# Performance work log

Hardware: AMD Instinct MI355X
Metric: run time of the kernel (lower is better)

Reference implementation:

```python
import jax, jax.numpy as jnp
import numpy as np

B, L, D_MODEL = 4, 1024, 512
D_STATE, EXPAND, D_CONV = 16, 2, 4
D_INNER = EXPAND * D_MODEL
DT_RANK = D_MODEL // 16
NUM_LAYERS = 2
NL2 = 2 * NUM_LAYERS  # at/vt layer pairs, index 2*i -> at_i, 2*i+1 -> vt_i


def setup_inputs() -> dict:
    key = jax.random.key(0)
    ks = jax.random.split(key, 16)
    s = 0.02
    inp = {
        'a_x': jax.random.normal(ks[0], (B, L, D_MODEL), jnp.float32),
        'v_x': jax.random.normal(ks[1], (B, L, D_MODEL), jnp.float32),
        't_x': jax.random.normal(ks[2], (B, L, D_MODEL), jnp.float32),
        'in_proj_w': s * jax.random.normal(ks[3], (NL2, 2 * D_INNER, D_MODEL), jnp.float32),
        'conv_w': s * jax.random.normal(ks[4], (NL2, 2, D_INNER, D_CONV), jnp.float32),
        'conv_b': jnp.zeros((NL2, 2, D_INNER), jnp.float32),
        'xproj_w': s * jax.random.normal(ks[5], (NL2, 2, DT_RANK + 2 * D_STATE, D_INNER), jnp.float32),
        'dtproj_w': s * jax.random.normal(ks[6], (NL2, 2, D_INNER, DT_RANK), jnp.float32),
        'dtproj_b': 0.1 * jax.random.normal(ks[7], (NL2, 2, D_INNER), jnp.float32),
        'A_log': jnp.log(jnp.broadcast_to(jnp.arange(1.0, D_STATE + 1.0, dtype=jnp.float32), (NL2, 2, D_INNER, D_STATE))),
        'Dskip': jnp.ones((NL2, 2, D_INNER), jnp.float32),
        'out_proj_w': s * jax.random.normal(ks[8], (NL2, D_MODEL, D_INNER), jnp.float32),
        'ln_w': jnp.ones((NL2, 2, D_MODEL), jnp.float32),
        'ln_b': jnp.zeros((NL2, 2, D_MODEL), jnp.float32),
    }
    return inp


def layer_norm(x, w, b, eps=1e-6):
    m = jnp.mean(x, -1, keepdims=True)
    v = jnp.var(x, -1, keepdims=True)
    return (x - m) * jax.lax.rsqrt(v + eps) * w + b


def causal_conv1d(x, w, b):
    # x: (B,L,d), depthwise causal conv with kernel w: (d,k), bias b: (d,)
    y = jax.lax.conv_general_dilated(
        x.transpose(0, 2, 1), w[:, None, :], (1,), [(D_CONV - 1, 0)],
        feature_group_count=D_INNER,
        dimension_numbers=('NCH', 'OIH', 'NCH'))
    return y.transpose(0, 2, 1) + b


def selective_scan(u, dt, A, Bm, Cm, Dskip):
    # u,dt:(B,L,d)  A:(d,N)  Bm,Cm:(B,L,N)  Dskip:(d,)
    dA = jnp.exp(dt[..., None] * A)                    # (B,L,d,N)
    dBu = (dt * u)[..., None] * Bm[:, :, None, :]      # (B,L,d,N)

    def step(h, inp):
        dA_t, dBu_t, C_t = inp
        h = dA_t * h + dBu_t                           # (B,d,N)
        return h, jnp.einsum('bdn,bn->bd', h, C_t)

    h0 = jnp.zeros((u.shape[0], u.shape[2], D_STATE), u.dtype)
    xs = (jnp.moveaxis(dA, 1, 0), jnp.moveaxis(dBu, 1, 0), jnp.moveaxis(Cm, 1, 0))
    _, ys = jax.lax.scan(step, h0, xs)
    return jnp.moveaxis(ys, 0, 1) + u * Dskip


def _one_dir(x, cw, cb, xpw, dpw, dpb, A_log, Dskip):
    xc = jax.nn.silu(causal_conv1d(x, cw, cb))
    proj = xc @ xpw.T                                  # (B,L,dt_rank+2N)
    dt_r, Bm, Cm = jnp.split(proj, [DT_RANK, DT_RANK + D_STATE], axis=-1)
    dt = jax.nn.softplus(dt_r @ dpw.T + dpb)
    A = -jnp.exp(A_log)
    return selective_scan(xc, dt, A, Bm, Cm, Dskip)


def _bimamba(u, i, p):
    xz = u @ p['in_proj_w'][i].T
    x, z = jnp.split(xz, 2, axis=-1)
    yf = _one_dir(x, p['conv_w'][i, 0], p['conv_b'][i, 0], p['xproj_w'][i, 0],
                  p['dtproj_w'][i, 0], p['dtproj_b'][i, 0], p['A_log'][i, 0], p['Dskip'][i, 0])
    yb = _one_dir(x[:, ::-1], p['conv_w'][i, 1], p['conv_b'][i, 1], p['xproj_w'][i, 1],
                  p['dtproj_w'][i, 1], p['dtproj_b'][i, 1], p['A_log'][i, 1], p['Dskip'][i, 1])[:, ::-1]
    y = (yf + yb) * jax.nn.silu(z)
    return y @ p['out_proj_w'][i].T


def _enc_layer(a, t, i, p):
    ao = _bimamba(a, i, p)
    to = _bimamba(t, i, p)
    a_out = a + layer_norm(ao, p['ln_w'][i, 0], p['ln_b'][i, 0])
    t_out = t + layer_norm(to, p['ln_w'][i, 1], p['ln_b'][i, 1])
    return a_out, t_out


def reference(a_x, v_x, t_x, in_proj_w, conv_w, conv_b, xproj_w, dtproj_w, dtproj_b,
              A_log, Dskip, out_proj_w, ln_w, ln_b):
    p = dict(in_proj_w=in_proj_w, conv_w=conv_w, conv_b=conv_b, xproj_w=xproj_w,
             dtproj_w=dtproj_w, dtproj_b=dtproj_b, A_log=A_log, Dskip=Dskip,
             out_proj_w=out_proj_w, ln_w=ln_w, ln_b=ln_b)
    a_out, v_out, t_out = a_x, v_x, t_x
    for i in range(NUM_LAYERS):
        a_out, t_at = _enc_layer(a_out, t_out, 2 * i, p)
        v_out, t_vt = _enc_layer(v_out, t_out, 2 * i + 1, p)
        t_out = (t_at + t_vt) / 2
    return (a_out, v_out, t_out)
```

## Files before the change

### kernel.cpp

```cpp
#include <hip/hip_runtime.h>
#include <cstddef>

constexpr int B_      = 4;
constexpr int L_      = 1024;
constexpr int DM      = 512;
constexpr int DS      = 16;
constexpr int DI      = 1024;
constexpr int DTR     = 32;
constexpr int TOK     = B_ * L_;
constexpr int NLAYERS = 2;

constexpr size_t XZB = 0;
constexpr size_t XCB = (size_t)4 * TOK * 2 * DI * 2;
constexpr size_t PRB = XCB + (size_t)8 * TOK * DI * 2;
constexpr size_t WIB = PRB + (size_t)8 * TOK * 64 * 4;
constexpr size_t WOB = WIB + (size_t)4 * 2 * DI * DM * 2;
constexpr size_t WXB = WOB + (size_t)4 * DM * DI * 2;
constexpr size_t WS_NEED_BF = WXB + (size_t)8 * 64 * DI * 2;
constexpr size_t DTB2 = WS_NEED_BF;
constexpr size_t WS_NEED_DT = DTB2 + (size_t)8 * TOK * DI * 2;

constexpr int NCH = 16;
constexpr size_t PP_BYTE = (size_t)8 * 4 * NCH * 1024 * DS * 2;

#if defined(__has_builtin)
#if __has_builtin(__builtin_amdgcn_exp2f)
#define FAST_EXP2(x) __builtin_amdgcn_exp2f(x)
#endif
#endif
#ifndef FAST_EXP2
#define FAST_EXP2(x) exp2f(x)
#endif

__device__ __forceinline__ float silu_f(float x) { return x / (1.f + __expf(-x)); }

__device__ __forceinline__ float bf2f(unsigned short u) {
    union { unsigned u; float f; } v; v.u = ((unsigned)u) << 16; return v.f;
}
__device__ __forceinline__ unsigned short f2bf(float f) {
    union { float f; unsigned u; } v; v.f = f;
    unsigned r = v.u + 0x7FFFu + ((v.u >> 16) & 1u);
    return (unsigned short)(r >> 16);
}
__device__ __forceinline__ float softplus_f(float x) {
    float e = exp2f(-fabsf(x) * 1.44269504f);
    return fmaxf(x, 0.f) + 0.69314718f * log2f(1.f + e);
}

__device__ __forceinline__ size_t ovmap(size_t byte) {
    return ((byte >> 11) << 12) + (byte & 2047);
}
__device__ __forceinline__ void st4bf(char* b, size_t bank, size_t e, float4 v) {
    ushort4 o;
    o.x = f2bf(v.x); o.y = f2bf(v.y); o.z = f2bf(v.z); o.w = f2bf(v.w);
    *(ushort4*)(b + ovmap(bank + e * 2)) = o;
}
__device__ __forceinline__ float4 ld4bf(const char* b, size_t bank, size_t e) {
    ushort4 u = *(const ushort4*)(b + ovmap(bank + e * 2));
    return make_float4(bf2f(u.x), bf2f(u.y), bf2f(u.z), bf2f(u.w));
}

using bf16x8 = __attribute__((ext_vector_type(8))) short;
using f32x4v = __attribute__((ext_vector_type(4))) float;
using f32x2  = __attribute__((ext_vector_type(2))) float;

__device__ __forceinline__ void stage8(unsigned short* dst, const float* src) {
    float4 v0 = *(const float4*)src;
    float4 v1 = *(const float4*)(src + 4);
    ushort4 o0, o1;
    o0.x = f2bf(v0.x); o0.y = f2bf(v0.y); o0.z = f2bf(v0.z); o0.w = f2bf(v0.w);
    o1.x = f2bf(v1.x); o1.y = f2bf(v1.y); o1.z = f2bf(v1.z); o1.w = f2bf(v1.w);
    *(ushort4*)dst = o0;
    *(ushort4*)(dst + 4) = o1;
}
__device__ __forceinline__ void stage8(unsigned short* dst, const unsigned short* src) {
    *(uint4*)dst = *(const uint4*)src;
}

template<int N, int K, int LDKA, int BM, int BN, int FM, int FN, int EPI,
         typename TA, typename TW, typename TC>
__device__ __forceinline__ void mfma_gemm(const TA* __restrict__ A,
                                          const TW* __restrict__ W,
                                          TC* __restrict__ C,
                                          const float* __restrict__ bias)
{
    constexpr int WC  = BN / (FN * 16);
    constexpr int LDA = 40;
    __shared__ unsigned short As[BM * LDA];
    __shared__ unsigned short Bs[BN * LDA];
    const int tid  = threadIdx.x;
    const int lane = tid & 63, wid = tid >> 6;
    const int wr = wid / WC, wc = wid % WC;
    const int row0 = blockIdx.y * BM, col0 = blockIdx.x * BN;

    f32x4v acc[FM][FN] = {};
    constexpr int AITER = BM * 4 / 256;
    constexpr int BITER = BN * 4 / 256;

    for (int k0 = 0; k0 < K; k0 += 32) {
#pragma unroll
        for (int i = 0; i < AITER; ++i) {
            int f = i * 256 + tid;
            int row = f >> 2, c8 = (f & 3) * 8;
            stage8(&As[row * LDA + c8], A + (size_t)(row0 + row) * LDKA + k0 + c8);
        }
#pragma unroll
        for (int i = 0; i < BITER; ++i) {
            int f = i * 256 + tid;
            int row = f >> 2, c8 = (f & 3) * 8;
            stage8(&Bs[row * LDA + c8], W + (size_t)(col0 + row) * K + k0 + c8);
        }
        __syncthreads();
        bf16x8 af[FM], bfr[FN];
#pragma unroll
        for (int m = 0; m < FM; ++m)
            af[m] = *(const bf16x8*)&As[(wr * FM * 16 + m * 16 + (lane & 15)) * LDA + (lane >> 4) * 8];
#pragma unroll
        for (int n = 0; n < FN; ++n)
            bfr[n] = *(const bf16x8*)&Bs[(wc * FN * 16 + n * 16 + (lane & 15)) * LDA + (lane >> 4) * 8];
#pragma unroll
        for (int m = 0; m < FM; ++m)
#pragma unroll
            for (int n = 0; n < FN; ++n)
                acc[m][n] = __builtin_amdgcn_mfma_f32_16x16x32_bf16(af[m], bfr[n], acc[m][n], 0, 0, 0);
        __syncthreads();
    }
#pragma unroll
    for (int m = 0; m < FM; ++m) {
#pragma unroll
        for (int n = 0; n < FN; ++n) {
            int r0 = row0 + wr * FM * 16 + m * 16 + (lane >> 4) * 4;
            int c  = col0 + wc * FN * 16 + n * 16 + (lane & 15);
#pragma unroll
            for (int v = 0; v < 4; ++v) {
                float val = acc[m][n][v];
                if constexpr (EPI == 1) val = softplus_f(val + bias[c]);
                if constexpr (sizeof(TC) == 4)
                    C[(size_t)(r0 + v) * N + c] = val;
                else
                    C[(size_t)(r0 + v) * N + c] = f2bf(val);
            }
        }
    }
}

__global__ __launch_bounds__(256)
void k_wcast(const float* __restrict__ w1, const float* __restrict__ w2,
             const float* __restrict__ w3, unsigned short* __restrict__ o1,
             unsigned short* __restrict__ o2, unsigned short* __restrict__ o3)
{
    constexpr int N1 = 4 * 2 * DI * DM;
    constexpr int N2 = 4 * DM * DI;
    constexpr int N3 = 8 * 64 * DI;
    constexpr int T4 = (N1 + N2 + N3) / 4;
    for (int i = blockIdx.x * 256 + threadIdx.x; i < T4; i += gridDim.x * 256) {
        int e = i * 4;
        const float* src; unsigned short* dst; int off;
        if (e < N1)           { src = w1; dst = o1; off = e; }
        else if (e < N1 + N2) { src = w2; dst = o2; off = e - N1; }
        else                  { src = w3; dst = o3; off = e - N1 - N2; }
        float4 v = *(const float4*)(src + off);
        ushort4 o;
        o.x = f2bf(v.x); o.y = f2bf(v.y); o.z = f2bf(v.z); o.w = f2bf(v.w);
        *(ushort4*)(dst + off) = o;
    }
}

template<typename TW>
__global__ __launch_bounds__(256)
void k_inproj(const float* __restrict__ pa, const float* __restrict__ pt,
              const float* __restrict__ pv, const TW* __restrict__ w_all,
              unsigned short* __restrict__ xz, int layer)
{
    int g = blockIdx.z;
    const float* A = (g == 0) ? pa : (g == 2) ? pv : pt;
    int li = 2 * layer + (g >> 1);
    mfma_gemm<2 * DI, DM, DM, 128, 128, 4, 4, 0, float, TW, unsigned short>(
        A, w_all + (size_t)li * (2 * DI) * DM, xz + (size_t)g * TOK * (2 * DI), nullptr);
}

template<typename TW>
__global__ __launch_bounds__(256)
void k_xproj(const unsigned short* __restrict__ xc, const TW* __restrict__ xpw,
             float* __restrict__ proj, int layer)
{
    int gd = blockIdx.z;
    int dir = gd & 1;
    int li = 2 * layer + (gd >> 2);
    mfma_gemm<64, DI, DI, 128, 64, 4, 2, 0, unsigned short, TW, float>(
        xc + (size_t)gd * TOK * DI,
        xpw + (size_t)(li * 2 + dir) * 64 * DI,
        proj + (size_t)gd * TOK * 64, nullptr);
}

template<typename TW>
__global__ __launch_bounds__(256)
void k_outproj(const unsigned short* __restrict__ xcbuf, const TW* __restrict__ opw,
               float* __restrict__ yo, int layer)
{
    int g = blockIdx.z;
    int li = 2 * layer + (g >> 1);
    mfma_gemm<DM, DI, DI, 128, 128, 4, 4, 0, unsigned short, TW, float>(
        xcbuf + (size_t)(2 * g) * TOK * DI,
        opw + (size_t)li * DM * DI,
        yo + (size_t)g * TOK * DM, nullptr);
}

__global__ __launch_bounds__(256)
void k_dtmm(const float* __restrict__ proj, const float* __restrict__ dpw,
            const float* __restrict__ dpb, unsigned short* __restrict__ dt, int layer)
{
    int gd = blockIdx.z, dir = gd & 1;
    int li = 2 * layer + (gd >> 2);
    mfma_gemm<DI, 32, 64, 128, 128, 4, 4, 1, float, float, unsigned short>(
        proj + (size_t)gd * TOK * 64,
        dpw + (size_t)(li * 2 + dir) * DI * DTR,
        dt + (size_t)gd * TOK * DI,
        dpb + (size_t)(li * 2 + dir) * DI);
}

__global__ __launch_bounds__(256)
void k_conv(const unsigned short* __restrict__ xz, const float* __restrict__ cw,
            const float* __restrict__ cb, unsigned short* __restrict__ xc, int layer)
{
    constexpr int TT = 64;
    const int gd = blockIdx.y;
    const int g = gd >> 1, dir = gd & 1;
    const int li = 2 * layer + (g >> 1);
    const int d = threadIdx.x * 4;
    const int wbase = (li * 2 + dir) * DI + d;
    float w[4][4];
    *(float4*)w[0] = *(const float4*)(cw + (size_t)(wbase + 0) * 4);
    *(float4*)w[1] = *(const float4*)(cw + (size_t)(wbase + 1) * 4);
    *(float4*)w[2] = *(const float4*)(cw + (size_t)(wbase + 2) * 4);
    *(float4*)w[3] = *(const float4*)(cw + (size_t)(wbase + 3) * 4);
    const float4 bias = *(const float4*)(cb + wbase);

    const int t0 = blockIdx.x * TT;
    const int b = t0 >> 10, tt0 = t0 & 1023;
    const unsigned short* xcol = xz + ((size_t)g * TOK + (size_t)(b << 10)) * (2 * DI) + d;
    unsigned short* ocol = xc + ((size_t)gd * TOK + t0) * DI + d;

    auto ldx = [&](int tt, float* o) {
        if (tt >= 0 && tt < L_) {
            ushort4 v = *(const ushort4*)(xcol + (size_t)tt * (2 * DI));
            o[0] = bf2f(v.x); o[1] = bf2f(v.y); o[2] = bf2f(v.z); o[3] = bf2f(v.w);
        } else {
            o[0] = 0.f; o[1] = 0.f; o[2] = 0.f; o[3] = 0.f;
        }
    };

    if (dir == 0) {
        float x3[4], x2[4], x1[4], x0[4];
        ldx(tt0 - 3, x3); ldx(tt0 - 2, x2); ldx(tt0 - 1, x1);
#pragma unroll 4
        for (int j = 0; j < TT; ++j) {
            ldx(tt0 + j, x0);
            float r0 = bias.x + w[0][0] * x3[0] + w[0][1] * x2[0] + w[0][2] * x1[0] + w[0][3] * x0[0];
            float r1 = bias.y + w[1][0] * x3[1] + w[1][1] * x2[1] + w[1][2] * x1[1] + w[1][3] * x0[1];
            float r2 = bias.z + w[2][0] * x3[2] + w[2][1] * x2[2] + w[2][2] * x1[2] + w[2][3] * x0[2];
            float r3 = bias.w + w[3][0] * x3[3] + w[3][1] * x2[3] + w[3][2] * x1[3] + w[3][3] * x0[3];
            ushort4 o;
            o.x = f2bf(silu_f(r0)); o.y = f2bf(silu_f(r1));
            o.z = f2bf(silu_f(r2)); o.w = f2bf(silu_f(r3));
            *(ushort4*)(ocol + (size_t)j * DI) = o;
#pragma unroll
            for (int c = 0; c < 4; ++c) { x3[c] = x2[c]; x2[c] = x1[c]; x1[c] = x0[c]; }
        }
    } else {
        float p1[4], p2[4], p3[4], x0[4];
        ldx(tt0 + TT, p1); ldx(tt0 + TT + 1, p2); ldx(tt0 + TT + 2, p3);
#pragma unroll 4
        for (int j = TT - 1; j >= 0; --j) {
            ldx(tt0 + j, x0);
            float r0 = bias.x + w[0][3] * x0[0] + w[0][2] * p1[0] + w[0][1] * p2[0] + w[0][0] * p3[0];
            float r1 = bias.y + w[1][3] * x0[1] + w[1][2] * p1[1] + w[1][1] * p2[1] + w[1][0] * p3[1];
            float r2 = bias.z + w[2][3] * x0[2] + w[2][2] * p1[2] + w[2][1] * p2[2] + w[2][0] * p3[2];
            float r3 = bias.w + w[3][3] * x0[3] + w[3][2] * p1[3] + w[3][1] * p2[3] + w[3][0] * p3[3];
            ushort4 o;
            o.x = f2bf(silu_f(r0)); o.y = f2bf(silu_f(r1));
            o.z = f2bf(silu_f(r2)); o.w = f2bf(silu_f(r3));
            *(ushort4*)(ocol + (size_t)j * DI) = o;
#pragma unroll
            for (int c = 0; c < 4; ++c) { p3[c] = p2[c]; p2[c] = p1[c]; p1[c] = x0[c]; }
        }
    }
}

template<bool PW, bool P3>
__device__ __forceinline__ void scan_core(
    unsigned short* __restrict__ xb, const unsigned short* __restrict__ db,
    const float* __restrict__ prb, unsigned short* us, unsigned short* ts,
    int lane, int q, int dir, f32x2 (&h2)[8], const float (&An2)[DS],
    float a_base, float& cumdt, float Dk)
{
    for (int sub = 0; sub < 4; ++sub) {
        const int s0 = q * 64 + sub * 16;
        const int tb0 = dir ? (1008 - s0) : s0;
#pragma unroll
        for (int i = 0; i < 2; ++i) {
            int f = i * 64 + lane;
            int row = f >> 3, c8 = (f & 7) * 8;
            *(uint4*)&us[row * 64 + c8] = *(const uint4*)(xb + (size_t)(tb0 + row) * DI + c8);
            *(uint4*)&ts[row * 64 + c8] = *(const uint4*)(db + (size_t)(tb0 + row) * DI + c8);
        }
        for (int j = 0; j < 16; ++j) {
            const int row = dir ? (15 - j) : j;
            const int t = tb0 + row;
            const float* prw = prb + (size_t)t * 64;
            float u   = bf2f(us[row * 64 + lane]);
            float dtv = bf2f(ts[row * 64 + lane]);
            float du = dtv * u;
            f32x2 du2 = {du, du};
            if constexpr (!P3) cumdt += dtv;
            f32x2 dA[8];
            if constexpr (PW) {
                float r  = FAST_EXP2(dtv * a_base);
                float r2 = r * r, r4 = r2 * r2, r8 = r4 * r4;
                f32x2 v2 = {r2, r2}, v4 = {r4, r4}, v8 = {r8, r8};
                dA[0] = f32x2{r, r2};
                dA[1] = dA[0] * v2;
                dA[2] = dA[0] * v4;
                dA[3] = dA[1] * v4;
                dA[4] = dA[0] * v8;
                dA[5] = dA[1] * v8;
                dA[6] = dA[2] * v8;
                dA[7] = dA[3] * v8;
            } else {
#pragma unroll
                for (int i2 = 0; i2 < 8; ++i2)
                    dA[i2] = f32x2{FAST_EXP2(dtv * An2[2 * i2]),
                                   FAST_EXP2(dtv * An2[2 * i2 + 1])};
            }
            f32x2 acc = {0.f, 0.f};
#pragma unroll
            for (int i2 = 0; i2 < 8; ++i2) {
                f32x2 Bv = *(const f32x2*)(prw + 32 + 2 * i2);
                h2[i2] = dA[i2] * h2[i2] + du2 * Bv;
                if constexpr (P3) {
                    f32x2 Cv = *(const f32x2*)(prw + 48 + 2 * i2);
                    acc += h2[i2] * Cv;
                }
            }
            if constexpr (P3)
                xb[(size_t)t * DI + lane] = f2bf(acc.x + acc.y + u * Dk);
        }
    }
}

template<bool PRE>
__global__ __launch_bounds__(256, 4)
void k_scan_p1(const unsigned short* __restrict__ xc, const float* __restrict__ proj,
               const unsigned short* __restrict__ dtb,
               const float* __restrict__ dpw, const float* __restrict__ dpb,
               const float* __restrict__ A_log, char* __restrict__ hsb, int layer)
{
    __shared__ unsigned short us[4][16 * 64];
    __shared__ unsigned short ts[PRE ? 4 : 1][PRE ? 16 * 64 : 1];
    const int tid = threadIdx.x, lane = tid & 63;
    const int wid = __builtin_amdgcn_readfirstlane(tid >> 6);
    const int chblk = blockIdx.x >> 2, qh = blockIdx.x & 3;
    const int q = qh * 4 + wid;
    const int b = blockIdx.y, gd = blockIdx.z;
    const int g = gd >> 1, dir = gd & 1;
    const int li = 2 * layer + (g >> 1);
    const int ch0 = chblk * 64;
    const int wl = (li * 2 + dir) * DI + ch0 + lane;

    float An2[DS];
    const float* Ap = A_log + (size_t)wl * DS;
#pragma unroll
    for (int n = 0; n < DS; ++n) An2[n] = -__expf(Ap[n]) * 1.44269504f;

    const unsigned short* xb = xc + ((size_t)gd * TOK + (size_t)b * L_) * DI + ch0;
    const unsigned short* db = dtb + ((size_t)gd * TOK + (size_t)b * L_) * DI + ch0;
    const float* prb = proj + ((size_t)gd * TOK + (size_t)b * L_) * 64;
    size_t e0 = ((((size_t)gd * 4 + b) * NCH + q) * 1024 + ch0 + lane) * DS;

    if constexpr (PRE) {
        const float a_base = An2[0];
        bool pw = true;
#pragma unroll
        for (int n = 1; n < DS; ++n)
            pw = pw && (fabsf(An2[n] - (n + 1) * a_base) <= 1e-4f * fabsf(An2[n]));
        f32x2 h2[8] = {};
        float cumdt = 0.f;
        if (pw)
            scan_core<true, false>((unsigned short*)xb, db, prb, us[wid], ts[wid],
                                   lane, q, dir, h2, An2, a_base, cumdt, 0.f);
        else
            scan_core<false, false>((unsigned short*)xb, db, prb, us[wid], ts[wid],
                                    lane, q, dir, h2, An2, a_base, cumdt, 0.f);
        f32x2 pp[8];
        if (pw) {
            float R  = FAST_EXP2(cumdt * a_base);
            float R2 = R * R, R4 = R2 * R2, R8 = R4 * R4;
            f32x2 v2 = {R2, R2}, v4 = {R4, R4}, v8 = {R8, R8};
            pp[0] = f32x2{R, R2};
            pp[1] = pp[0] * v2; pp[2] = pp[0] * v4; pp[3] = pp[1] * v4;
            pp[4] = pp[0] * v8; pp[5] = pp[1] * v8; pp[6] = pp[2] * v8; pp[7] = pp[3] * v8;
        } else {
#pragma unroll
            for (int i2 = 0; i2 < 8; ++i2)
                pp[i2] = f32x2{FAST_EXP2(cumdt * An2[2 * i2]),
                               FAST_EXP2(cumdt * An2[2 * i2 + 1])};
        }
#pragma unroll
        for (int n = 0; n < DS; n += 4) {
            st4bf(hsb, 0, e0 + n, make_float4(h2[n / 2].x, h2[n / 2].y,
                                              h2[n / 2 + 1].x, h2[n / 2 + 1].y));
            st4bf(hsb, PP_BYTE, e0 + n, make_float4(pp[n / 2].x, pp[n / 2].y,
                                                    pp[n / 2 + 1].x, pp[n / 2 + 1].y));
        }
    } else {
        float w[DTR];
        const float* wp = dpw + (size_t)wl * DTR;
#pragma unroll
        for (int k = 0; k < DTR; ++k) w[k] = wp[k];
        const float bias = dpb[wl];
        float h[DS];
#pragma unroll
        for (int n = 0; n < DS; ++n) h[n] = 0.f;
        float cumdt = 0.f;
        for (int sub = 0; sub < 4; ++sub) {
            const int s0 = q * 64 + sub * 16;
            const int tb0 = dir ? (1008 - s0) : s0;
#pragma unroll
            for (int i = 0; i < 2; ++i) {
                int f = i * 64 + lane;
                int row = f >> 3, c8 = (f & 7) * 8;
                *(uint4*)&us[wid][row * 64 + c8] = *(const uint4*)(xb + (size_t)(tb0 + row) * DI + c8);
            }
            for (int j = 0; j < 16; ++j) {
                const int row = dir ? (15 - j) : j;
                const int t = tb0 + row;
                const float* prw = prb + (size_t)t * 64;
                float u = bf2f(us[wid][row * 64 + lane]);
                float a0 = bias;
#pragma unroll
                for (int k4 = 0; k4 < 8; ++k4) {
                    float4 p = *(const float4*)(prw + k4 * 4);
                    a0 += w[k4 * 4 + 0] * p.x + w[k4 * 4 + 1] * p.y
                        + w[k4 * 4 + 2] * p.z + w[k4 * 4 + 3] * p.w;
                }
                float dtv = softplus_f(a0);
                float du = dtv * u;
                cumdt += dtv;
#pragma unroll
                for (int n = 0; n < DS; ++n) {
                    float e = exp2f(dtv * An2[n]);
                    h[n] = e * h[n] + du * prw[32 + n];
                }
            }
        }
#pragma unroll
        for (int n = 0; n < DS; n += 4) {
            st4bf(hsb, 0, e0 + n, make_float4(h[n], h[n + 1], h[n + 2], h[n + 3]));
            float4 cp = make_float4(exp2f(cumdt * An2[n]),     exp2f(cumdt * An2[n + 1]),
                                    exp2f(cumdt * An2[n + 2]), exp2f(cumdt * An2[n + 3]));
            st4bf(hsb, PP_BYTE, e0 + n, cp);
        }
    }
}

__global__ __launch_bounds__(256)
void k_scan_p2(char* __restrict__ hsb)
{
    const int ch = blockIdx.x * 256 + threadIdx.x;
    const int b = blockIdx.y, gd = blockIdx.z;
    float h[DS];
#pragma unroll
    for (int n = 0; n < DS; ++n) h[n] = 0.f;
    for (int q = 0; q < NCH; ++q) {
        size_t e0 = ((((size_t)gd * 4 + b) * NCH + q) * 1024 + ch) * DS;
#pragma unroll
        for (int n = 0; n < DS; n += 4) {
            float4 hl = ld4bf(hsb, 0, e0 + n);
            float4 pp = ld4bf(hsb, PP_BYTE, e0 + n);
            st4bf(hsb, 0, e0 + n, make_float4(h[n], h[n + 1], h[n + 2], h[n + 3]));
            h[n + 0] = pp.x * h[n + 0] + hl.x;
            h[n + 1] = pp.y * h[n + 1] + hl.y;
            h[n + 2] = pp.z * h[n + 2] + hl.z;
            h[n + 3] = pp.w * h[n + 3] + hl.w;
        }
    }
}

template<bool PRE>
__global__ __launch_bounds__(256, 4)
void k_scan_p3(unsigned short* __restrict__ xc, const float* __restrict__ proj,
               const unsigned short* __restrict__ dtb,
               const float* __restrict__ dpw, const float* __restrict__ dpb,
               const float* __restrict__ A_log, const float* __restrict__ Dskip,
               const char* __restrict__ hsb, int layer)
{
    __shared__ unsigned short us[4][16 * 64];
    __shared__ unsigned short ts[PRE ? 4 : 1][PRE ? 16 * 64 : 1];
    const int tid = threadIdx.x, lane = tid & 63;
    const int wid = __builtin_amdgcn_readfirstlane(tid >> 6);
    const int chblk = blockIdx.x >> 2, qh = blockIdx.x & 3;
    const int q = qh * 4 + wid;
    const int b = blockIdx.y, gd = blockIdx.z;
    const int g = gd >> 1, dir = gd & 1;
    const int li = 2 * layer + (g >> 1);
    const int ch0 = chblk * 64;
    const int wl = (li * 2 + dir) * DI + ch0 + lane;

    float An2[DS];
    const float* Ap = A_log + (size_t)wl * DS;
#pragma unroll
    for (int n = 0; n < DS; ++n) An2[n] = -__expf(Ap[n]) * 1.44269504f;
    const float Dk = Dskip[wl];

    unsigned short* xb = xc + ((size_t)gd * TOK + (size_t)b * L_) * DI + ch0;
    const unsigned short* db = dtb + ((size_t)gd * TOK + (size_t)b * L_) * DI + ch0;
    const float* prb = proj + ((size_t)gd * TOK + (size_t)b * L_) * 64;
    size_t e0 = ((((size_t)gd * 4 + b) * NCH + q) * 1024 + ch0 + lane) * DS;

    if constexpr (PRE) {
        const float a_base = An2[0];
        bool pw = true;
#pragma unroll
        for (int n = 1; n < DS; ++n)
            pw = pw && (fabsf(An2[n] - (n + 1) * a_base) <= 1e-4f * fabsf(An2[n]));
        f32x2 h2[8];
#pragma unroll
        for (int n = 0; n < DS; n += 4) {
            float4 v = ld4bf(hsb, 0, e0 + n);
            h2[n / 2]     = f32x2{v.x, v.y};
            h2[n / 2 + 1] = f32x2{v.z, v.w};
        }
        float cumdt = 0.f;
        if (pw)
            scan_core<true, true>(xb, db, prb, us[wid], ts[wid],
                                  lane, q, dir, h2, An2, a_base, cumdt, Dk);
        else
            scan_core<false, true>(xb, db, prb, us[wid], ts[wid],
                                   lane, q, dir, h2, An2, a_base, cumdt, Dk);
    } else {
        float w[DTR];
        const float* wp = dpw + (size_t)wl * DTR;
#pragma unroll
        for (int k = 0; k < DTR; ++k) w[k] = wp[k];
        const float bias = dpb[wl];
        float h[DS];
#pragma unroll
        for (int n = 0; n < DS; n += 4) {
            float4 v = ld4bf(hsb, 0, e0 + n);
            h[n] = v.x; h[n + 1] = v.y; h[n + 2] = v.z; h[n + 3] = v.w;
        }
        for (int sub = 0; sub < 4; ++sub) {
            const int s0 = q * 64 + sub * 16;
            const int tb0 = dir ? (1008 - s0) : s0;
#pragma unroll
            for (int i = 0; i < 2; ++i) {
                int f = i * 64 + lane;
                int row = f >> 3, c8 = (f & 7) * 8;
                *(uint4*)&us[wid][row * 64 + c8] = *(const uint4*)(xb + (size_t)(tb0 + row) * DI + c8);
            }
            for (int j = 0; j < 16; ++j) {
                const int row = dir ? (15 - j) : j;
                const int t = tb0 + row;
                const float* prw = prb + (size_t)t * 64;
                float u = bf2f(us[wid][row * 64 + lane]);
                float a0 = bias;
#pragma unroll
                for (int k4 = 0; k4 < 8; ++k4) {
                    float4 p = *(const float4*)(prw + k4 * 4);
                    a0 += w[k4 * 4 + 0] * p.x + w[k4 * 4 + 1] * p.y
                        + w[k4 * 4 + 2] * p.z + w[k4 * 4 + 3] * p.w;
                }
                float dtv = softplus_f(a0);
                float du = dtv * u;
                float acc = 0.f;
#pragma unroll
                for (int n = 0; n < DS; ++n) {
                    float e = exp2f(dtv * An2[n]);
                    h[n] = e * h[n] + du * prw[32 + n];
                    acc += h[n] * prw[48 + n];
                }
                xb[(size_t)t * DI + lane] = f2bf(acc + u * Dk);
            }
        }
    }
}

__global__ __launch_bounds__(256)
void k_combine(unsigned short* __restrict__ xcbuf, const unsigned short* __restrict__ xz)
{
    int g = blockIdx.y;
    size_t idx = ((size_t)blockIdx.x * 256 + threadIdx.x) * 4;
    size_t m = idx >> 10, d = idx & 1023;
    unsigned short* yf_p = xcbuf + (size_t)(2 * g) * TOK * DI + idx;
    const unsigned short* yb_p = xcbuf + (size_t)(2 * g + 1) * TOK * DI + idx;
    const unsigned short* z_p  = xz + ((size_t)g * TOK + m) * (2 * DI) + DI + d;
    ushort4 yf = *(const ushort4*)yf_p;
    ushort4 yb = *(const ushort4*)yb_p;
    ushort4 zz = *(const ushort4*)z_p;
    ushort4 o;
    o.x = f2bf((bf2f(yf.x) + bf2f(yb.x)) * silu_f(bf2f(zz.x)));
    o.y = f2bf((bf2f(yf.y) + bf2f(yb.y)) * silu_f(bf2f(zz.y)));
    o.z = f2bf((bf2f(yf.z) + bf2f(yb.z)) * silu_f(bf2f(zz.z)));
    o.w = f2bf((bf2f(yf.w) + bf2f(yb.w)) * silu_f(bf2f(zz.w)));
    *(ushort4*)yf_p = o;
}

__device__ __forceinline__ void blk_red2(float& a, float& b, float* red)
{
#pragma unroll
    for (int o = 32; o; o >>= 1) {
        a += __shfl_down(a, o);
        b += __shfl_down(b, o);
    }
    int lane = threadIdx.x & 63, wid = threadIdx.x >> 6;
    if (lane == 0) { red[wid] = a; red[4 + wid] = b; }
    __syncthreads();
    a = red[0] + red[1] + red[2] + red[3];
    b = red[4] + red[5] + red[6] + red[7];
    __syncthreads();
}

__global__ __launch_bounds__(256)
void k_ln(const float* __restrict__ yo, const float* __restrict__ lnw,
          const float* __restrict__ lnb, const float* __restrict__ resA,
          const float* __restrict__ resT, const float* __restrict__ resV,
          float* __restrict__ outA, float* __restrict__ outT,
          float* __restrict__ outV, int layer)
{
    int tok = blockIdx.x, tid = threadIdx.x;
    __shared__ float red[8];
    float t1a = 0.f, t1b = 0.f;
#pragma unroll
    for (int s = 0; s < 4; ++s) {
        const float* p = yo + ((size_t)s * TOK + tok) * DM;
        float x0 = p[tid], x1 = p[tid + 256];
        float sm = x0 + x1, sq = x0 * x0 + x1 * x1;
        blk_red2(sm, sq, red);
        float mean = sm * (1.f / 512.f);
        float var  = sq * (1.f / 512.f) - mean * mean;
        float rstd = rsqrtf(var + 1e-6f);
        int li = 2 * layer + (s >> 1);
        int half = s & 1;
        const float* wv = lnw + (size_t)(li * 2 + half) * DM;
        const float* bv = lnb + (size_t)(li * 2 + half) * DM;
        float v0 = (x0 - mean) * rstd * wv[tid] + bv[tid];
        float v1 = (x1 - mean) * rstd * wv[tid + 256] + bv[tid + 256];
        size_t o0 = (size_t)tok * DM + tid, o1 = o0 + 256;
        if (s == 0) {
            outA[o0] = resA[o0] + v0;
            outA[o1] = resA[o1] + v1;
        } else if (s == 1) {
            t1a = v0; t1b = v1;
        } else if (s == 2) {
            outV[o0] = resV[o0] + v0;
            outV[o1] = resV[o1] + v1;
        } else {
            outT[o0] = resT[o0] + 0.5f * (t1a + v0);
            outT[o1] = resT[o1] + 0.5f * (t1b + v1);
        }
    }
}

extern "C" void kernel_launch(void* const* d_in, const int* in_sizes, int n_in,
                              void* d_out, int out_size, void* d_ws, size_t ws_size,
                              hipStream_t stream)
{
    (void)in_sizes; (void)n_in; (void)out_size;
    const float* a_x       = (const float*)d_in[0];
    const float* v_x       = (const float*)d_in[1];
    const float* t_x       = (const float*)d_in[2];
    const float* in_proj_w = (const float*)d_in[3];
    const float* conv_w    = (const float*)d_in[4];
    const float* conv_b    = (const float*)d_in[5];
    const float* xproj_w   = (const float*)d_in[6];
    const float* dtproj_w  = (const float*)d_in[7];
    const float* dtproj_b  = (const float*)d_in[8];
    const float* A_log     = (const float*)d_in[9];
    const float* Dskip     = (const float*)d_in[10];
    const float* out_proj_w= (const float*)d_in[11];
    const float* ln_w      = (const float*)d_in[12];
    const float* ln_b      = (const float*)d_in[13];

    char* wsb = (char*)d_ws;
    unsigned short* xz   = (unsigned short*)(wsb + XZB);
    unsigned short* xc   = (unsigned short*)(wsb + XCB);
    float*          proj = (float*)(wsb + PRB);
    float*          yo   = (float*)(wsb + XZB);
    char*           hsb  = wsb + XZB;
    unsigned short* wib  = (unsigned short*)(wsb + WIB);
    unsigned short* wob  = (unsigned short*)(wsb + WOB);
    unsigned short* wxb  = (unsigned short*)(wsb + WXB);
    unsigned short* dtb  = (unsigned short*)(wsb + DTB2);

    const bool wbf = (ws_size >= WS_NEED_BF);
    const bool pre = (ws_size >= WS_NEED_DT);

    float* out   = (float*)d_out;
    float* slotA = out;
    float* slotV = out + (size_t)TOK * DM;
    float* slotT = out + (size_t)2 * TOK * DM;

    if (wbf)
        k_wcast<<<dim3(1024), 256, 0, stream>>>(in_proj_w, out_proj_w, xproj_w,
                                                wib, wob, wxb);

    for (int layer = 0; layer < NLAYERS; ++layer) {
        const float* sa = layer ? slotA : a_x;
        const float* st = layer ? slotT : t_x;
        const float* sv = layer ? slotV : v_x;

        if (wbf)
            k_inproj<unsigned short><<<dim3(16, 32, 4), 256, 0, stream>>>(
                sa, st, sv, wib, xz, layer);
        else
            k_inproj<float><<<dim3(16, 32, 4), 256, 0, stream>>>(
                sa, st, sv, in_proj_w, xz, layer);

        k_conv<<<dim3(64, 8), 256, 0, stream>>>(xz, conv_w, conv_b, xc, layer);

        if (wbf)
            k_xproj<unsigned short><<<dim3(1, 32, 8), 256, 0, stream>>>(
                xc, wxb, proj, layer);
        else
            k_xproj<float><<<dim3(1, 32, 8), 256, 0, stream>>>(
                xc, xproj_w, proj, layer);

        if (pre) {
            k_dtmm<<<dim3(8, 32, 8), 256, 0, stream>>>(proj, dtproj_w, dtproj_b,
                                                       dtb, layer);
            k_scan_p1<true><<<dim3(64, 4, 8), 256, 0, stream>>>(
                xc, proj, dtb, dtproj_w, dtproj_b, A_log, hsb, layer);
            k_scan_p2<<<dim3(4, 4, 8), 256, 0, stream>>>(hsb);
            k_scan_p3<true><<<dim3(64, 4, 8), 256, 0, stream>>>(
                xc, proj, dtb, dtproj_w, dtproj_b, A_log, Dskip, hsb, layer);
        } else {
            k_scan_p1<false><<<dim3(64, 4, 8), 256, 0, stream>>>(
                xc, proj, dtb, dtproj_w, dtproj_b, A_log, hsb, layer);
            k_scan_p2<<<dim3(4, 4, 8), 256, 0, stream>>>(hsb);
            k_scan_p3<false><<<dim3(64, 4, 8), 256, 0, stream>>>(
                xc, proj, dtb, dtproj_w, dtproj_b, A_log, Dskip, hsb, layer);
        }

        k_combine<<<dim3(4096, 4), 256, 0, stream>>>(xc, xz);

        if (wbf)
            k_outproj<unsigned short><<<dim3(4, 32, 4), 256, 0, stream>>>(
                xc, wob, yo, layer);
        else
            k_outproj<float><<<dim3(4, 32, 4), 256, 0, stream>>>(
                xc, out_proj_w, yo, layer);

        k_ln<<<dim3(4096), 256, 0, stream>>>(yo, ln_w, ln_b, sa, st, sv,
                                             slotA, slotT, slotV, layer);
    }
}
```

Baseline: 750.3 us.

## Software-pipeline scan tile loads and stage B/C rows in shared memory

The scan core now prefetches the next 16-step tile of u, dt and B/C projections into registers while computing the current one, then commits them to LDS. B and C values are read from a per-wave LDS buffer instead of per-step global loads. Scan direction becomes a template parameter and the inner step loop is fully unrolled. The fast-path predicate is made wave-uniform with __all. The aim is to hide global-load latency in the sequential scan, at the cost of more registers and extra LDS.

```diff
diff --git a/kernel.cpp b/kernel.cpp
--- a/kernel.cpp
+++ b/kernel.cpp
@@ -287,27 +287,50 @@
     }
 }
 
-template<bool PW, bool P3>
-__device__ __forceinline__ void scan_core(
+template<int NF, bool PW, bool P3, int DIR>
+__device__ __forceinline__ void scan_core2(
     unsigned short* __restrict__ xb, const unsigned short* __restrict__ db,
-    const float* __restrict__ prb, unsigned short* us, unsigned short* ts,
-    int lane, int q, int dir, f32x2 (&h2)[8], const float (&An2)[DS],
-    float a_base, float& cumdt, float Dk)
-{
+    const float* __restrict__ prb, unsigned short* __restrict__ us,
+    unsigned short* __restrict__ ts, float* __restrict__ bc,
+    const int lane, const int q, f32x2 (&h2)[8], const float (&An2)[DS],
+    const float a_base, float& cumdt, const float Dk)
+{
+    constexpr int PB = NF / 16;
+    const int rowu = lane >> 3, c8u = (lane & 7) * 8;
+    const int rowB = lane >> 2, cB = (lane & 3) * (PB * 4);
+
+    uint4 pu[2], pt[2]; float4 pb[PB];
+
+    auto ISSUE = [&](int sub) {
+        const int s0 = q * 64 + sub * 16;
+        const int tb0 = DIR ? (1008 - s0) : s0;
+        pu[0] = *(const uint4*)(xb + (size_t)(tb0 + rowu) * DI + c8u);
+        pu[1] = *(const uint4*)(xb + (size_t)(tb0 + 8 + rowu) * DI + c8u);
+        pt[0] = *(const uint4*)(db + (size_t)(tb0 + rowu) * DI + c8u);
+        pt[1] = *(const uint4*)(db + (size_t)(tb0 + 8 + rowu) * DI + c8u);
+        const float* pr = prb + (size_t)(tb0 + rowB) * 64 + 32 + cB;
+        pb[0] = *(const float4*)pr;
+        if constexpr (PB == 2) pb[1] = *(const float4*)(pr + 4);
+    };
+    auto COMMIT = [&]() {
+        *(uint4*)&us[rowu * 64 + c8u]       = pu[0];
+        *(uint4*)&us[(8 + rowu) * 64 + c8u] = pu[1];
+        *(uint4*)&ts[rowu * 64 + c8u]       = pt[0];
+        *(uint4*)&ts[(8 + rowu) * 64 + c8u] = pt[1];
+        *(float4*)&bc[rowB * NF + cB] = pb[0];
+        if constexpr (PB == 2) *(float4*)&bc[rowB * NF + cB + 4] = pb[1];
+    };
+
+    ISSUE(0);
     for (int sub = 0; sub < 4; ++sub) {
+        COMMIT();
+        if (sub < 3) ISSUE(sub + 1);
         const int s0 = q * 64 + sub * 16;
-        const int tb0 = dir ? (1008 - s0) : s0;
-#pragma unroll
-        for (int i = 0; i < 2; ++i) {
-            int f = i * 64 + lane;
-            int row = f >> 3, c8 = (f & 7) * 8;
-            *(uint4*)&us[row * 64 + c8] = *(const uint4*)(xb + (size_t)(tb0 + row) * DI + c8);
-            *(uint4*)&ts[row * 64 + c8] = *(const uint4*)(db + (size_t)(tb0 + row) * DI + c8);
-        }
+        const int tb0 = DIR ? (1008 - s0) : s0;
+#pragma unroll
         for (int j = 0; j < 16; ++j) {
-            const int row = dir ? (15 - j) : j;
+            const int row = DIR ? (15 - j) : j;
             const int t = tb0 + row;
-            const float* prw = prb + (size_t)t * 64;
             float u   = bf2f(us[row * 64 + lane]);
             float dtv = bf2f(ts[row * 64 + lane]);
             float du = dtv * u;
@@ -332,13 +355,14 @@
                     dA[i2] = f32x2{FAST_EXP2(dtv * An2[2 * i2]),
                                    FAST_EXP2(dtv * An2[2 * i2 + 1])};
             }
+            const float* Brow = &bc[row * NF];
             f32x2 acc = {0.f, 0.f};
 #pragma unroll
             for (int i2 = 0; i2 < 8; ++i2) {
-                f32x2 Bv = *(const f32x2*)(prw + 32 + 2 * i2);
+                f32x2 Bv = *(const f32x2*)(Brow + 2 * i2);
                 h2[i2] = dA[i2] * h2[i2] + du2 * Bv;
                 if constexpr (P3) {
-                    f32x2 Cv = *(const f32x2*)(prw + 48 + 2 * i2);
+                    f32x2 Cv = *(const f32x2*)(Brow + 16 + 2 * i2);
                     acc += h2[i2] * Cv;
                 }
             }
@@ -357,6 +381,7 @@
 {
     __shared__ unsigned short us[4][16 * 64];
     __shared__ unsigned short ts[PRE ? 4 : 1][PRE ? 16 * 64 : 1];
+    __shared__ float bcs[PRE ? 4 : 1][PRE ? 16 * 16 : 1];
     const int tid = threadIdx.x, lane = tid & 63;
     const int wid = __builtin_amdgcn_readfirstlane(tid >> 6);
     const int chblk = blockIdx.x >> 2, qh = blockIdx.x & 3;
@@ -379,18 +404,29 @@
 
     if constexpr (PRE) {
         const float a_base = An2[0];
-        bool pw = true;
+        bool pwl = true;
 #pragma unroll
         for (int n = 1; n < DS; ++n)
-            pw = pw && (fabsf(An2[n] - (n + 1) * a_base) <= 1e-4f * fabsf(An2[n]));
+            pwl = pwl && (fabsf(An2[n] - (n + 1) * a_base) <= 1e-4f * fabsf(An2[n]));
+        const bool pw = __all(pwl);
         f32x2 h2[8] = {};
         float cumdt = 0.f;
-        if (pw)
-            scan_core<true, false>((unsigned short*)xb, db, prb, us[wid], ts[wid],
-                                   lane, q, dir, h2, An2, a_base, cumdt, 0.f);
-        else
-            scan_core<false, false>((unsigned short*)xb, db, prb, us[wid], ts[wid],
-                                    lane, q, dir, h2, An2, a_base, cumdt, 0.f);
+        unsigned short* xbm = (unsigned short*)xb;
+        if (pw) {
+            if (dir == 0)
+                scan_core2<16, true, false, 0>(xbm, db, prb, us[wid], ts[wid], bcs[wid],
+                                               lane, q, h2, An2, a_base, cumdt, 0.f);
+            else
+                scan_core2<16, true, false, 1>(xbm, db, prb, us[wid], ts[wid], bcs[wid],
+                                               lane, q, h2, An2, a_base, cumdt, 0.f);
+        } else {
+            if (dir == 0)
+                scan_core2<16, false, false, 0>(xbm, db, prb, us[wid], ts[wid], bcs[wid],
+                                                lane, q, h2, An2, a_base, cumdt, 0.f);
+            else
+                scan_core2<16, false, false, 1>(xbm, db, prb, us[wid], ts[wid], bcs[wid],
+                                                lane, q, h2, An2, a_base, cumdt, 0.f);
+        }
         f32x2 pp[8];
         if (pw) {
             float R  = FAST_EXP2(cumdt * a_base);
@@ -496,6 +532,7 @@
 {
     __shared__ unsigned short us[4][16 * 64];
     __shared__ unsigned short ts[PRE ? 4 : 1][PRE ? 16 * 64 : 1];
+    __shared__ float bcs[PRE ? 4 : 1][PRE ? 16 * 32 : 1];
     const int tid = threadIdx.x, lane = tid & 63;
     const int wid = __builtin_amdgcn_readfirstlane(tid >> 6);
     const int chblk = blockIdx.x >> 2, qh = blockIdx.x & 3;
@@ -519,10 +556,11 @@
 
     if constexpr (PRE) {
         const float a_base = An2[0];
-        bool pw = true;
+        bool pwl = true;
 #pragma unroll
         for (int n = 1; n < DS; ++n)
-            pw = pw && (fabsf(An2[n] - (n + 1) * a_base) <= 1e-4f * fabsf(An2[n]));
+            pwl = pwl && (fabsf(An2[n] - (n + 1) * a_base) <= 1e-4f * fabsf(An2[n]));
+        const bool pw = __all(pwl);
         f32x2 h2[8];
 #pragma unroll
         for (int n = 0; n < DS; n += 4) {
@@ -531,12 +569,21 @@
             h2[n / 2 + 1] = f32x2{v.z, v.w};
         }
         float cumdt = 0.f;
-        if (pw)
-            scan_core<true, true>(xb, db, prb, us[wid], ts[wid],
-                                  lane, q, dir, h2, An2, a_base, cumdt, Dk);
-        else
-            scan_core<false, true>(xb, db, prb, us[wid], ts[wid],
-                                   lane, q, dir, h2, An2, a_base, cumdt, Dk);
+        if (pw) {
+            if (dir == 0)
+                scan_core2<32, true, true, 0>(xb, db, prb, us[wid], ts[wid], bcs[wid],
+                                              lane, q, h2, An2, a_base, cumdt, Dk);
+            else
+                scan_core2<32, true, true, 1>(xb, db, prb, us[wid], ts[wid], bcs[wid],
+                                              lane, q, h2, An2, a_base, cumdt, Dk);
+        } else {
+            if (dir == 0)
+                scan_core2<32, false, true, 0>(xb, db, prb, us[wid], ts[wid], bcs[wid],
+                                               lane, q, h2, An2, a_base, cumdt, Dk);
+            else
+                scan_core2<32, false, true, 1>(xb, db, prb, us[wid], ts[wid], bcs[wid],
+                                               lane, q, h2, An2, a_base, cumdt, Dk);
+        }
     } else {
         float w[DTR];
         const float* wp = dpw + (size_t)wl * DTR;
```

Measured after the change: 845.1 us. 1.13x slower.
